# Performance work log

Measured on AMD Instinct MI355X. Metric: run time of the kernel, lower is better.

## Reference

```python
import jax, jax.numpy as jnp
import numpy as np

B, L, C = 32, 128, 21
PATCH, STRIDE = 16, 16
E, H, HEADS = 128, 128, 8
NLAYERS = 2
KSIZE = 3
PRED = 96
N = (L - PATCH) // STRIDE + 1  # 8 patches


def setup_inputs() -> dict:
    key = jax.random.key(0)
    ks = jax.random.split(key, 24)
    g = lambda i, shape, s=0.05: jax.random.normal(ks[i], shape, jnp.float32) * s
    return {
        'x': g(0, (B, L, C), 1.0),
        'embed_W': g(1, (E, PATCH)), 'embed_b': g(2, (E,)),
        'ln_g': jnp.ones((E,), jnp.float32), 'ln_b': jnp.zeros((E,), jnp.float32),
        'qW': g(3, (E, E)), 'qb': g(4, (E,)),
        'kW': g(5, (E, E)), 'kb': g(6, (E,)),
        'vW': g(7, (E, E)), 'vb': g(8, (E,)),
        'lstm_Wx': g(9, (NLAYERS, 4 * H, E)), 'lstm_Wh': g(10, (NLAYERS, 4 * H, H)), 'lstm_b': g(11, (NLAYERS, 4 * H)),
        'conv_W': g(12, (E, E, KSIZE)), 'conv_b': g(13, (E,)),
        'ssm_W': g(14, (E, E)), 'ssm_b': g(15, (E,)),
        'outp_W': g(16, (E, E)), 'outp_b': g(17, (E,)),
        'proj_W': g(18, (PRED, E)), 'proj_b': g(19, (PRED,)),
    }


def _layernorm(x, g, b, eps=1e-5):
    m = x.mean(-1, keepdims=True)
    v = ((x - m) ** 2).mean(-1, keepdims=True)
    return (x - m) * jax.lax.rsqrt(v + eps) * g + b


def _xlstm_dqn(ctx, Wx, Wh, bias):
    # DQNxLSTM: re-runs a 2-layer LSTM over the FULL sequence L times,
    # carrying (h,c) across iterations; returns the outputs of the last pass.
    ctx_T = jnp.swapaxes(ctx, 0, 1)  # [N, Bc, E]
    Bc = ctx.shape[0]
    h0 = jnp.zeros((NLAYERS, Bc, H), ctx.dtype)
    c0 = jnp.zeros_like(h0)

    def cell(carry, x_t):  # x_t: [Bc, E]
        h, c = carry
        inp = x_t
        hs, cs = [], []
        for l in range(NLAYERS):
            gates = inp @ Wx[l].T + h[l] @ Wh[l].T + bias[l]  # [Bc, 4H]
            i, f, g_, o = jnp.split(gates, 4, axis=-1)
            c_new = jax.nn.sigmoid(f) * c[l] + jax.nn.sigmoid(i) * jnp.tanh(g_)
            h_new = jax.nn.sigmoid(o) * jnp.tanh(c_new)
            hs.append(h_new); cs.append(c_new)
            inp = h_new
        return (jnp.stack(hs), jnp.stack(cs)), inp

    def outer(carry, _):
        carry2, outs = jax.lax.scan(cell, carry, ctx_T)  # outs: [N, Bc, H]
        return carry2, outs

    _, all_outs = jax.lax.scan(outer, (h0, c0), None, length=N)
    return jnp.swapaxes(all_outs[-1], 0, 1)  # [Bc, N, H]


def _conv1d_same(x, W, b):  # x: [Bc, N, E]
    y = jax.lax.conv_general_dilated(
        jnp.swapaxes(x, 1, 2), W, (1,), 'SAME',
        dimension_numbers=('NCH', 'OIH', 'NCH'))
    return jnp.swapaxes(y + b[None, :, None], 1, 2)


def reference(x, embed_W, embed_b, ln_g, ln_b, qW, qb, kW, kb, vW, vb,
              lstm_Wx, lstm_Wh, lstm_b, conv_W, conv_b, ssm_W, ssm_b,
              outp_W, outp_b, proj_W, proj_b):
    Bc = B * C
    # channel independence: b l c -> (b c) l
    xc = jnp.swapaxes(x, 1, 2).reshape(Bc, L)
    # patching (unfold)
    idx = jnp.arange(N)[:, None] * STRIDE + jnp.arange(PATCH)[None, :]
    patches = xc[:, idx]  # [Bc, N, PATCH]
    emb = patches @ embed_W.T + embed_b  # [Bc, N, E]
    xn = _layernorm(emb, ln_g, ln_b)
    # attention (faithful to original, incl. scale by sqrt(E) and bhnl,bhnd->bhnd einsum)
    d = E // HEADS
    q = (xn @ qW.T + qb).reshape(Bc, N, HEADS, d).transpose(0, 2, 1, 3)
    k = (xn @ kW.T + kb).reshape(Bc, N, HEADS, d).transpose(0, 2, 1, 3)
    v = (xn @ vW.T + vb).reshape(Bc, N, HEADS, d).transpose(0, 2, 1, 3)
    attn = jax.nn.softmax(jnp.einsum('bhnd,bhld->bhnl', q, k) / (E ** 0.5), axis=-1)
    ctx = jnp.einsum('bhnl,bhnd->bhnd', attn, v)  # as in original (elementwise-in-n)
    ctx = ctx.transpose(0, 2, 1, 3).reshape(Bc, N, E)
    ctx = _xlstm_dqn(ctx, lstm_Wx, lstm_Wh, lstm_b)
    ctx = _conv1d_same(ctx, conv_W, conv_b)
    ctx = ctx @ ssm_W.T + ssm_b
    ctx = ctx @ outp_W.T + outp_b
    ctx = ctx + xn  # residual onto the normed input (as in original)
    y = ctx @ proj_W.T + proj_b  # [Bc, N, PRED]
    return y
```

## Files before the change

### kernel.cpp

```cpp
#include <hip/hip_runtime.h>

typedef unsigned short ushort_t;
typedef unsigned int uint_t;

using bf16x8 = __attribute__((ext_vector_type(8))) short;
using f32x4  = __attribute__((ext_vector_type(4))) float;

__device__ __forceinline__ ushort_t f2b(float f){
    union { float f; uint_t u; } v; v.f = f;
    uint_t u = v.u;
    uint_t r = (u + 0x7FFFu + ((u >> 16) & 1u)) >> 16;
    return (ushort_t)r;
}

__global__ void prep_k(const float* __restrict__ vW, const float* __restrict__ Wx,
                       const float* __restrict__ Wh, const float* __restrict__ cW,
                       const float* __restrict__ sW, const float* __restrict__ oW,
                       const float* __restrict__ pW, const float* __restrict__ x,
                       ushort_t* __restrict__ wb, float* __restrict__ xT)
{
    int idx = blockIdx.x * 256 + threadIdx.x;
    switch (blockIdx.y){
    case 0: if (idx < 16384) wb[idx]          = f2b(vW[idx]);           break;
    case 1: if (idx < 65536) wb[16384  + idx] = f2b(Wx[idx]);           break;
    case 2: if (idx < 65536) wb[81920  + idx] = f2b(Wh[idx]);           break;
    case 3: if (idx < 65536) wb[147456 + idx] = f2b(Wx[65536 + idx]);   break;
    case 4: if (idx < 65536) wb[212992 + idx] = f2b(Wh[65536 + idx]);   break;
    case 5: if (idx < 49152){
                int k = idx >> 14; int oi = idx & 16383;
                wb[278528 + idx] = f2b(cW[oi * 3 + k]);
            } break;
    case 6: if (idx < 16384) wb[327680 + idx] = f2b(sW[idx]);           break;
    case 7: if (idx < 16384) wb[344064 + idx] = f2b(oW[idx]);           break;
    case 8: if (idx < 12288) wb[360448 + idx] = f2b(pW[idx]);           break;
    case 9:
        for (int i = idx; i < 86016; i += 65536){
            int bc = i >> 7, l = i & 127;
            int b = bc / 21, c = bc % 21;
            xT[i] = x[(b * 128 + l) * 21 + c];
        }
        break;
    }
}

__global__ __launch_bounds__(256) void head_k(
    const float* __restrict__ xT, const float* __restrict__ eW,
    const float* __restrict__ eb, const float* __restrict__ lng,
    const float* __restrict__ lnb, const ushort_t* __restrict__ vWb,
    const float* __restrict__ vb, const ushort_t* __restrict__ wx0b,
    const float* __restrict__ lb, float* __restrict__ xnF, float* __restrict__ X0F)
{
    __shared__ ushort_t xnL[2048];
    __shared__ ushort_t c0L[2048];

    const int tid = threadIdx.x;
    const int wv = tid >> 6, lane = tid & 63;
    const int rowbase = blockIdx.x * 16;
    const int e0 = lane, e1 = lane + 64;

    float w0[16], w1[16];
#pragma unroll
    for (int p = 0; p < 16; ++p){ w0[p] = eW[e0 * 16 + p]; w1[p] = eW[e1 * 16 + p]; }
    const float bi0 = eb[e0], bi1 = eb[e1];
    const float ga0 = lng[e0], ga1 = lng[e1];
    const float be0 = lnb[e0], be1 = lnb[e1];

    for (int i = wv; i < 16; i += 4){
        const int row = rowbase + i;
        const int bc = row >> 3, n = row & 7;
        const float* xp = xT + bc * 128 + n * 16;
        float v0 = bi0, v1 = bi1;
#pragma unroll
        for (int p = 0; p < 16; ++p){
            float pv = xp[p];
            v0 += w0[p] * pv; v1 += w1[p] * pv;
        }
        float s = v0 + v1, sq = v0 * v0 + v1 * v1;
#pragma unroll
        for (int m = 32; m >= 1; m >>= 1){
            s  += __shfl_xor(s,  m);
            sq += __shfl_xor(sq, m);
        }
        float mean = s * (1.f / 128.f);
        float var  = sq * (1.f / 128.f) - mean * mean;
        float r    = rsqrtf(var + 1e-5f);
        float y0 = (v0 - mean) * r * ga0 + be0;
        float y1 = (v1 - mean) * r * ga1 + be1;
        xnF[row * 128 + e0] = y0;
        xnF[row * 128 + e1] = y1;
        const int sz = (i & 7) << 3;
        xnL[i * 128 + (e0 ^ sz)] = f2b(y0);
        xnL[i * 128 + (e1 ^ sz)] = f2b(y1);
    }
    __syncthreads();

    const int r0 = lane & 15, g = lane >> 4, sw = r0 & 7;
    bf16x8 a[4];
#pragma unroll
    for (int kt = 0; kt < 4; ++kt)
        a[kt] = *(const bf16x8*)(&xnL[r0 * 128 + ((kt * 32 + g * 8) ^ (sw << 3))]);

#pragma unroll
    for (int j = 0; j < 2; ++j){
        const int nt = wv * 2 + j;
        const int col = nt * 16 + r0;
        float bv = vb[col];
        f32x4 acc = {bv, bv, bv, bv};
#pragma unroll
        for (int kt = 0; kt < 4; ++kt)
            acc = __builtin_amdgcn_mfma_f32_16x16x32_bf16(
                    a[kt], *(const bf16x8*)(vWb + col * 128 + kt * 32 + g * 8), acc, 0, 0, 0);
#pragma unroll
        for (int q = 0; q < 4; ++q){
            int rr = g * 4 + q;
            c0L[rr * 128 + (col ^ ((rr & 7) << 3))] = f2b(acc[q]);
        }
    }
    __syncthreads();

#pragma unroll
    for (int kt = 0; kt < 4; ++kt)
        a[kt] = *(const bf16x8*)(&c0L[r0 * 128 + ((kt * 32 + g * 8) ^ (sw << 3))]);

#pragma unroll
    for (int j = 0; j < 8; ++j){
        const int nt = wv * 8 + j;
        const int col = nt * 16 + r0;
        float bv = lb[col];
        f32x4 acc = {bv, bv, bv, bv};
#pragma unroll
        for (int kt = 0; kt < 4; ++kt)
            acc = __builtin_amdgcn_mfma_f32_16x16x32_bf16(
                    a[kt], *(const bf16x8*)(wx0b + col * 128 + kt * 32 + g * 8), acc, 0, 0, 0);
#pragma unroll
        for (int q = 0; q < 4; ++q)
            X0F[(rowbase + g * 4 + q) * 512 + col] = acc[q];
    }
}

__global__ __launch_bounds__(512, 2) void lstm_f2(
    const float* __restrict__ X0, const ushort_t* __restrict__ Wh0,
    const ushort_t* __restrict__ Wx1, const ushort_t* __restrict__ Wh1,
    const float* __restrict__ lb, ushort_t* __restrict__ outB)
{
    extern __shared__ ushort_t smem[];
    ushort_t* hbuf = smem;
    ushort_t* wxs  = smem + 8192;

    const int tid = threadIdx.x;
    const int wid = tid >> 6, lane = tid & 63;
    const int r0 = lane & 15, g = lane >> 4;
    const int sw = r0 & 7;
    const int bcb = blockIdx.x * 16;
    const float K1 = 1.44269504f, K2 = 2.88539008f;

    for (int i = tid; i < 8192; i += 512) hbuf[i] = 0;
    for (int idx = tid; idx < 8192; idx += 512){
        int col = idx >> 4, c = idx & 15;
        *(bf16x8*)(wxs + col * 128 + ((c ^ (col & 7)) << 3)) =
            *(const bf16x8*)(Wx1 + col * 128 + c * 8);
    }

    bf16x8 wh0[4][4], wh1[4][4];
#pragma unroll
    for (int t4 = 0; t4 < 4; ++t4){
        const int cb = t4 * 128 + wid * 16;
#pragma unroll
        for (int kt = 0; kt < 4; ++kt){
            wh0[t4][kt] = *(const bf16x8*)(Wh0 + (cb + r0) * 128 + kt * 32 + g * 8);
            wh1[t4][kt] = *(const bf16x8*)(Wh1 + (cb + r0) * 128 + kt * 32 + g * 8);
        }
    }
    float b1v[4];
#pragma unroll
    for (int t4 = 0; t4 < 4; ++t4) b1v[t4] = lb[512 + t4 * 128 + wid * 16 + r0];

    const char* adr[4];
#pragma unroll
    for (int kt = 0; kt < 4; ++kt)
        adr[kt] = (const char*)hbuf + r0 * 256 + (((kt * 32 + g * 8) ^ (sw << 3)) << 1);
    char* wrq[4];
#pragma unroll
    for (int q = 0; q < 4; ++q){
        int row = g * 4 + q;
        wrq[q] = (char*)hbuf + row * 256 + (((wid * 16 + r0) ^ ((row & 7) << 3)) << 1);
    }
    const char* wxp[4][2];
    {
        const int e = (sw >> 2) * 64;
#pragma unroll
        for (int t4 = 0; t4 < 4; ++t4){
            const char* base = (const char*)wxs
                + (t4 * 128 + wid * 16 + r0) * 256 + ((g ^ (sw & 3)) * 16);
            wxp[t4][0] = base + e;
            wxp[t4][1] = base + (64 - e);
        }
    }
    const char* xp[4];
#pragma unroll
    for (int q = 0; q < 4; ++q)
        xp[q] = (const char*)(X0 + (bcb + g * 4 + q) * 4096 + wid * 16 + r0) + 2048;
    int tnn = 1;

    float c0[4] = {0,0,0,0}, c1[4] = {0,0,0,0};

    f32x4 acc[4];
#pragma unroll
    for (int t4 = 0; t4 < 4; ++t4)
#pragma unroll
        for (int q = 0; q < 4; ++q)
            acc[t4][q] = *(const float*)(xp[q] - 2048 + t4 * 512);

    __syncthreads();

#pragma unroll 1
    for (int tt = 0; tt < 32; ++tt){
#pragma unroll
        for (int pp = 0; pp < 2; ++pp){
            const int ph = tt * 2 + pp;
            const int RDO = (pp ^ 1) * 4096;
            const int WRO = pp * 4096;

            bf16x8 a0[4], ah[4];
#pragma unroll
            for (int kt = 0; kt < 4; ++kt){
                a0[kt] = *(const bf16x8*)(adr[kt] + RDO);
                ah[kt] = *(const bf16x8*)(adr[kt] + 8192 + RDO);
            }

#pragma unroll
            for (int kt = 0; kt < 4; ++kt)
#pragma unroll
                for (int t4 = 0; t4 < 4; ++t4)
                    acc[t4] = __builtin_amdgcn_mfma_f32_16x16x32_bf16(a0[kt], wh0[t4][kt], acc[t4], 0, 0, 0);

#pragma unroll
            for (int q = 0; q < 4; ++q){
                float iv = acc[0][q], fv = acc[1][q], gv = acc[2][q], ov = acc[3][q];
                float af = 1.f + __builtin_amdgcn_exp2f(-K1 * fv);
                float ai = 1.f + __builtin_amdgcn_exp2f(-K1 * iv);
                float bg = 1.f + __builtin_amdgcn_exp2f( K2 * gv);
                float cn = c0[q] * __builtin_amdgcn_rcpf(af)
                         + (bg - 2.f) * __builtin_amdgcn_rcpf(ai * bg);
                c0[q] = cn;
                float ao = 1.f + __builtin_amdgcn_exp2f(-K1 * ov);
                float bc = 1.f + __builtin_amdgcn_exp2f( K2 * cn);
                float hv = (bc - 2.f) * __builtin_amdgcn_rcpf(ao * bc);
                *(ushort_t*)(wrq[q] + WRO) = f2b(hv);
            }

            if (ph > 0){
                f32x4 accB[4];
#pragma unroll
                for (int t4 = 0; t4 < 4; ++t4){
                    f32x4 tmp = {b1v[t4], b1v[t4], b1v[t4], b1v[t4]};
                    accB[t4] = tmp;
                }
#pragma unroll
                for (int kt = 0; kt < 4; ++kt)
#pragma unroll
                    for (int t4 = 0; t4 < 4; ++t4){
                        bf16x8 wx = *(const bf16x8*)(wxp[t4][kt & 1] + ((kt >> 1) << 7));
                        accB[t4] = __builtin_amdgcn_mfma_f32_16x16x32_bf16(a0[kt], wx,          accB[t4], 0, 0, 0);
                        accB[t4] = __builtin_amdgcn_mfma_f32_16x16x32_bf16(ah[kt], wh1[t4][kt], accB[t4], 0, 0, 0);
                    }
#pragma unroll
                for (int q = 0; q < 4; ++q){
                    float iv = accB[0][q], fv = accB[1][q], gv = accB[2][q], ov = accB[3][q];
                    float af = 1.f + __builtin_amdgcn_exp2f(-K1 * fv);
                    float ai = 1.f + __builtin_amdgcn_exp2f(-K1 * iv);
                    float bg = 1.f + __builtin_amdgcn_exp2f( K2 * gv);
                    float cn = c1[q] * __builtin_amdgcn_rcpf(af)
                             + (bg - 2.f) * __builtin_amdgcn_rcpf(ai * bg);
                    c1[q] = cn;
                    float ao = 1.f + __builtin_amdgcn_exp2f(-K1 * ov);
                    float bc = 1.f + __builtin_amdgcn_exp2f( K2 * cn);
                    float hv = (bc - 2.f) * __builtin_amdgcn_rcpf(ao * bc);
                    *(ushort_t*)(wrq[q] + 8192 + WRO) = f2b(hv);
                    if (ph >= 57){
                        int row = g * 4 + q;
                        outB[((bcb + row) * 8 + ((ph - 1) & 7)) * 128 + wid * 16 + r0] = f2b(hv);
                    }
                }
            }

            if (ph < 63){
#pragma unroll
                for (int t4 = 0; t4 < 4; ++t4)
#pragma unroll
                    for (int q = 0; q < 4; ++q)
                        acc[t4][q] = *(const float*)(xp[q] + t4 * 512);
                long d = (tnn == 7) ? -14336L : 2048L;
                tnn = (tnn == 7) ? 0 : tnn + 1;
#pragma unroll
                for (int q = 0; q < 4; ++q) xp[q] += d;
            }
            __syncthreads();
        }
    }

    {
        bf16x8 a0[4], ah[4];
#pragma unroll
        for (int kt = 0; kt < 4; ++kt){
            a0[kt] = *(const bf16x8*)(adr[kt] + 4096);
            ah[kt] = *(const bf16x8*)(adr[kt] + 8192 + 4096);
        }
        f32x4 acc2[4];
#pragma unroll
        for (int t4 = 0; t4 < 4; ++t4){
            f32x4 tmp = {b1v[t4], b1v[t4], b1v[t4], b1v[t4]};
            acc2[t4] = tmp;
        }
#pragma unroll
        for (int kt = 0; kt < 4; ++kt)
#pragma unroll
            for (int t4 = 0; t4 < 4; ++t4){
                bf16x8 wx = *(const bf16x8*)(wxp[t4][kt & 1] + ((kt >> 1) << 7));
                acc2[t4] = __builtin_amdgcn_mfma_f32_16x16x32_bf16(a0[kt], wx,          acc2[t4], 0, 0, 0);
                acc2[t4] = __builtin_amdgcn_mfma_f32_16x16x32_bf16(ah[kt], wh1[t4][kt], acc2[t4], 0, 0, 0);
            }
#pragma unroll
        for (int q = 0; q < 4; ++q){
            float iv = acc2[0][q], fv = acc2[1][q], gv = acc2[2][q], ov = acc2[3][q];
            float af = 1.f + __builtin_amdgcn_exp2f(-K1 * fv);
            float ai = 1.f + __builtin_amdgcn_exp2f(-K1 * iv);
            float bg = 1.f + __builtin_amdgcn_exp2f( K2 * gv);
            float cn = c1[q] * __builtin_amdgcn_rcpf(af)
                     + (bg - 2.f) * __builtin_amdgcn_rcpf(ai * bg);
            float ao = 1.f + __builtin_amdgcn_exp2f(-K1 * ov);
            float bc = 1.f + __builtin_amdgcn_exp2f( K2 * cn);
            float hv = (bc - 2.f) * __builtin_amdgcn_rcpf(ao * bc);
            int row = g * 4 + q;
            outB[((bcb + row) * 8 + 7) * 128 + wid * 16 + r0] = f2b(hv);
        }
    }
}

__global__ __launch_bounds__(256) void tail_k(
    const ushort_t* __restrict__ ls, const ushort_t* __restrict__ cWk,
    const float* __restrict__ cbias, const ushort_t* __restrict__ sW,
    const float* __restrict__ sbias, const ushort_t* __restrict__ oW,
    const float* __restrict__ obias, const float* __restrict__ xnF,
    const ushort_t* __restrict__ pW, const float* __restrict__ pbias,
    float* __restrict__ out)
{
    __shared__ ushort_t bufA[2048];
    __shared__ ushort_t bufB[2048];
    const int tid = threadIdx.x;
    const int wv = tid >> 6, lane = tid & 63;
    const int r0 = lane & 15, g = lane >> 4;
    const int rowbase = blockIdx.x * 16;

    {
        const int n = r0 & 7;
        bf16x8 a[3][4];
#pragma unroll
        for (int k = 0; k < 3; ++k){
            bool valid = (n + k >= 1) && (n + k <= 8);
            const ushort_t* ap = ls + (rowbase + r0 + k - 1) * 128 + g * 8;
#pragma unroll
            for (int kt = 0; kt < 4; ++kt){
                bf16x8 z = {0,0,0,0,0,0,0,0};
                a[k][kt] = valid ? *(const bf16x8*)(ap + kt * 32) : z;
            }
        }
#pragma unroll
        for (int j = 0; j < 2; ++j){
            const int nt = wv * 2 + j;
            const int col = nt * 16 + r0;
            float bv = cbias[col];
            f32x4 acc = {bv, bv, bv, bv};
#pragma unroll
            for (int k = 0; k < 3; ++k)
#pragma unroll
                for (int kt = 0; kt < 4; ++kt)
                    acc = __builtin_amdgcn_mfma_f32_16x16x32_bf16(
                            a[k][kt], *(const bf16x8*)(cWk + k * 16384 + col * 128 + kt * 32 + g * 8),
                            acc, 0, 0, 0);
#pragma unroll
            for (int q = 0; q < 4; ++q){
                int row = g * 4 + q;
                bufA[row * 128 + (col ^ ((row & 7) << 3))] = f2b(acc[q]);
            }
        }
    }
    __syncthreads();
    {
        bf16x8 a[4];
#pragma unroll
        for (int kt = 0; kt < 4; ++kt)
            a[kt] = *(const bf16x8*)(&bufA[r0 * 128 + ((kt * 32 + g * 8) ^ ((r0 & 7) << 3))]);
#pragma unroll
        for (int j = 0; j < 2; ++j){
            const int nt = wv * 2 + j;
            const int col = nt * 16 + r0;
            float bv = sbias[col];
            f32x4 acc = {bv, bv, bv, bv};
#pragma unroll
            for (int kt = 0; kt < 4; ++kt)
                acc = __builtin_amdgcn_mfma_f32_16x16x32_bf16(
                        a[kt], *(const bf16x8*)(sW + col * 128 + kt * 32 + g * 8), acc, 0, 0, 0);
#pragma unroll
            for (int q = 0; q < 4; ++q){
                int row = g * 4 + q;
                bufB[row * 128 + (col ^ ((row & 7) << 3))] = f2b(acc[q]);
            }
        }
    }
    __syncthreads();
    {
        bf16x8 a[4];
#pragma unroll
        for (int kt = 0; kt < 4; ++kt)
            a[kt] = *(const bf16x8*)(&bufB[r0 * 128 + ((kt * 32 + g * 8) ^ ((r0 & 7) << 3))]);
#pragma unroll
        for (int j = 0; j < 2; ++j){
            const int nt = wv * 2 + j;
            const int col = nt * 16 + r0;
            float bv = obias[col];
            f32x4 acc = {bv, bv, bv, bv};
#pragma unroll
            for (int kt = 0; kt < 4; ++kt)
                acc = __builtin_amdgcn_mfma_f32_16x16x32_bf16(
                        a[kt], *(const bf16x8*)(oW + col * 128 + kt * 32 + g * 8), acc, 0, 0, 0);
#pragma unroll
            for (int q = 0; q < 4; ++q){
                int row = g * 4 + q;
                float v = acc[q] + xnF[(rowbase + row) * 128 + col];
                bufA[row * 128 + (col ^ ((row & 7) << 3))] = f2b(v);
            }
        }
    }
    __syncthreads();
    {
        bf16x8 a[4];
#pragma unroll
        for (int kt = 0; kt < 4; ++kt)
            a[kt] = *(const bf16x8*)(&bufA[r0 * 128 + ((kt * 32 + g * 8) ^ ((r0 & 7) << 3))]);
        for (int nt = wv; nt < 6; nt += 4){
            const int col = nt * 16 + r0;
            float bv = pbias[col];
            f32x4 acc = {bv, bv, bv, bv};
#pragma unroll
            for (int kt = 0; kt < 4; ++kt)
                acc = __builtin_amdgcn_mfma_f32_16x16x32_bf16(
                        a[kt], *(const bf16x8*)(pW + col * 128 + kt * 32 + g * 8), acc, 0, 0, 0);
#pragma unroll
            for (int q = 0; q < 4; ++q)
                out[(rowbase + g * 4 + q) * 96 + col] = acc[q];
        }
    }
}

extern "C" void kernel_launch(void* const* d_in, const int* in_sizes, int n_in,
                              void* d_out, int out_size, void* d_ws, size_t ws_size,
                              hipStream_t stream)
{
    const float* x   = (const float*)d_in[0];
    const float* eW  = (const float*)d_in[1];
    const float* eb  = (const float*)d_in[2];
    const float* lng = (const float*)d_in[3];
    const float* lnb = (const float*)d_in[4];
    const float* vW  = (const float*)d_in[9];
    const float* vb  = (const float*)d_in[10];
    const float* Wx  = (const float*)d_in[11];
    const float* Wh  = (const float*)d_in[12];
    const float* lb  = (const float*)d_in[13];
    const float* cW  = (const float*)d_in[14];
    const float* cb_ = (const float*)d_in[15];
    const float* sW  = (const float*)d_in[16];
    const float* sb  = (const float*)d_in[17];
    const float* oW  = (const float*)d_in[18];
    const float* ob  = (const float*)d_in[19];
    const float* pW  = (const float*)d_in[20];
    const float* pb  = (const float*)d_in[21];

    char* ws = (char*)d_ws;
    float*    xnF = (float*)   (ws + 0);
    float*    X0F = (float*)   (ws + 5505024);
    ushort_t* lsB = (ushort_t*)(ws + 16515072);
    ushort_t* wb  = (ushort_t*)(ws + 17891328);
    float*    xT  = (float*)   (ws + 18874368);

    hipFuncSetAttribute((const void*)lstm_f2,
                        hipFuncAttributeMaxDynamicSharedMemorySize, 147456);

    prep_k<<<dim3(256, 10), 256, 0, stream>>>(vW, Wx, Wh, cW, sW, oW, pW, x, wb, xT);
    head_k<<<336, 256, 0, stream>>>(xT, eW, eb, lng, lnb, wb + 0, vb, wb + 16384, lb,
                                    xnF, X0F);
    lstm_f2<<<42, 512, 147456, stream>>>(X0F, wb + 81920, wb + 147456, wb + 212992,
                                         lb, lsB);
    tail_k<<<336, 256, 0, stream>>>(lsB, wb + 278528, cb_, wb + 327680, sb,
                                    wb + 344064, ob, xnF, wb + 360448, pb, (float*)d_out);
}
```

Measured before the change: 174.5 us.

## Fuse weight prep and input transpose into head kernel, convert head weights inline

Merges the separate prep kernel into the head kernel. Extra blocks (336..511) convert the LSTM, conv, ssm, out and proj weights to bf16 while the first 336 blocks run the embedding, layernorm and projections. The head blocks now gather their input columns straight into shared memory instead of reading a pre-transposed buffer, and they convert vW and Wx[0] to bf16 on the fly with packed convert instructions. This removes one kernel launch and the intermediate xT round trip through global memory. In exchange, each head block re-converts its fp32 weights itself, reading twice the bytes from global memory.

```diff
diff --git a/kernel.cpp b/kernel.cpp
--- a/kernel.cpp
+++ b/kernel.cpp
@@ -12,52 +12,64 @@
     uint_t r = (u + 0x7FFFu + ((u >> 16) & 1u)) >> 16;
     return (ushort_t)r;
 }
-
-__global__ void prep_k(const float* __restrict__ vW, const float* __restrict__ Wx,
-                       const float* __restrict__ Wh, const float* __restrict__ cW,
-                       const float* __restrict__ sW, const float* __restrict__ oW,
-                       const float* __restrict__ pW, const float* __restrict__ x,
-                       ushort_t* __restrict__ wb, float* __restrict__ xT)
+__device__ __forceinline__ uint_t cvtpk(float lo, float hi){
+    uint_t r;
+    asm("v_cvt_pk_bf16_f32 %0, %1, %2" : "=v"(r) : "v"(lo), "v"(hi));
+    return r;
+}
+__device__ __forceinline__ bf16x8 ldcvt8(const float* p){
+    float4 a = *(const float4*)p;
+    float4 b = *(const float4*)(p + 4);
+    union { uint_t u[4]; bf16x8 v; } r;
+    r.u[0] = cvtpk(a.x, a.y); r.u[1] = cvtpk(a.z, a.w);
+    r.u[2] = cvtpk(b.x, b.y); r.u[3] = cvtpk(b.z, b.w);
+    return r.v;
+}
+
+__global__ __launch_bounds__(256) void headprep_k(
+    const float* __restrict__ x, const float* __restrict__ eW,
+    const float* __restrict__ eb, const float* __restrict__ lng,
+    const float* __restrict__ lnb, const float* __restrict__ vW,
+    const float* __restrict__ vb, const float* __restrict__ Wx,
+    const float* __restrict__ Wh, const float* __restrict__ cW,
+    const float* __restrict__ sW, const float* __restrict__ oW,
+    const float* __restrict__ pW, const float* __restrict__ lb,
+    ushort_t* __restrict__ wb, float* __restrict__ xnF, float* __restrict__ X0F)
 {
-    int idx = blockIdx.x * 256 + threadIdx.x;
-    switch (blockIdx.y){
-    case 0: if (idx < 16384) wb[idx]          = f2b(vW[idx]);           break;
-    case 1: if (idx < 65536) wb[16384  + idx] = f2b(Wx[idx]);           break;
-    case 2: if (idx < 65536) wb[81920  + idx] = f2b(Wh[idx]);           break;
-    case 3: if (idx < 65536) wb[147456 + idx] = f2b(Wx[65536 + idx]);   break;
-    case 4: if (idx < 65536) wb[212992 + idx] = f2b(Wh[65536 + idx]);   break;
-    case 5: if (idx < 49152){
-                int k = idx >> 14; int oi = idx & 16383;
-                wb[278528 + idx] = f2b(cW[oi * 3 + k]);
-            } break;
-    case 6: if (idx < 16384) wb[327680 + idx] = f2b(sW[idx]);           break;
-    case 7: if (idx < 16384) wb[344064 + idx] = f2b(oW[idx]);           break;
-    case 8: if (idx < 12288) wb[360448 + idx] = f2b(pW[idx]);           break;
-    case 9:
-        for (int i = idx; i < 86016; i += 65536){
-            int bc = i >> 7, l = i & 127;
-            int b = bc / 21, c = bc % 21;
-            xT[i] = x[(b * 128 + l) * 21 + c];
-        }
-        break;
-    }
-}
-
-__global__ __launch_bounds__(256) void head_k(
-    const float* __restrict__ xT, const float* __restrict__ eW,
-    const float* __restrict__ eb, const float* __restrict__ lng,
-    const float* __restrict__ lnb, const ushort_t* __restrict__ vWb,
-    const float* __restrict__ vb, const ushort_t* __restrict__ wx0b,
-    const float* __restrict__ lb, float* __restrict__ xnF, float* __restrict__ X0F)
-{
+    __shared__ float    xcolL[256];
     __shared__ ushort_t xnL[2048];
     __shared__ ushort_t c0L[2048];
 
     const int tid = threadIdx.x;
+
+    if (blockIdx.x >= 336){
+        const int stride = 176 * 256;
+        for (int i = (blockIdx.x - 336) * 256 + tid; i < 290816; i += stride){
+            if (i < 65536)       wb[81920  + i]            = f2b(Wh[i]);
+            else if (i < 131072) wb[147456 + (i - 65536)]  = f2b(Wx[65536 + (i - 65536)]);
+            else if (i < 196608) wb[212992 + (i - 131072)] = f2b(Wh[65536 + (i - 131072)]);
+            else if (i < 245760){
+                int j = i - 196608; int k = j >> 14, oi = j & 16383;
+                wb[278528 + j] = f2b(cW[oi * 3 + k]);
+            }
+            else if (i < 262144) wb[327680 + (i - 245760)] = f2b(sW[i - 245760]);
+            else if (i < 278528) wb[344064 + (i - 262144)] = f2b(oW[i - 262144]);
+            else                 wb[360448 + (i - 278528)] = f2b(pW[i - 278528]);
+        }
+        return;
+    }
+
     const int wv = tid >> 6, lane = tid & 63;
     const int rowbase = blockIdx.x * 16;
+
+    {
+        const int colw = tid >> 7, l = tid & 127;
+        const int bcs = blockIdx.x * 2 + colw;
+        const int bs = bcs / 21, cs = bcs % 21;
+        xcolL[colw * 128 + l] = x[(bs * 128 + l) * 21 + cs];
+    }
+
     const int e0 = lane, e1 = lane + 64;
-
     float w0[16], w1[16];
 #pragma unroll
     for (int p = 0; p < 16; ++p){ w0[p] = eW[e0 * 16 + p]; w1[p] = eW[e1 * 16 + p]; }
@@ -65,10 +77,11 @@
     const float ga0 = lng[e0], ga1 = lng[e1];
     const float be0 = lnb[e0], be1 = lnb[e1];
 
+    __syncthreads();
+
     for (int i = wv; i < 16; i += 4){
         const int row = rowbase + i;
-        const int bc = row >> 3, n = row & 7;
-        const float* xp = xT + bc * 128 + n * 16;
+        const float* xp = &xcolL[(i >> 3) * 128 + (i & 7) * 16];
         float v0 = bi0, v1 = bi1;
 #pragma unroll
         for (int p = 0; p < 16; ++p){
@@ -109,7 +122,7 @@
 #pragma unroll
         for (int kt = 0; kt < 4; ++kt)
             acc = __builtin_amdgcn_mfma_f32_16x16x32_bf16(
-                    a[kt], *(const bf16x8*)(vWb + col * 128 + kt * 32 + g * 8), acc, 0, 0, 0);
+                    a[kt], ldcvt8(vW + col * 128 + kt * 32 + g * 8), acc, 0, 0, 0);
 #pragma unroll
         for (int q = 0; q < 4; ++q){
             int rr = g * 4 + q;
@@ -131,7 +144,7 @@
 #pragma unroll
         for (int kt = 0; kt < 4; ++kt)
             acc = __builtin_amdgcn_mfma_f32_16x16x32_bf16(
-                    a[kt], *(const bf16x8*)(wx0b + col * 128 + kt * 32 + g * 8), acc, 0, 0, 0);
+                    a[kt], ldcvt8(Wx + col * 128 + kt * 32 + g * 8), acc, 0, 0, 0);
 #pragma unroll
         for (int q = 0; q < 4; ++q)
             X0F[(rowbase + g * 4 + q) * 512 + col] = acc[q];
@@ -481,14 +494,12 @@
     float*    X0F = (float*)   (ws + 5505024);
     ushort_t* lsB = (ushort_t*)(ws + 16515072);
     ushort_t* wb  = (ushort_t*)(ws + 17891328);
-    float*    xT  = (float*)   (ws + 18874368);
 
     hipFuncSetAttribute((const void*)lstm_f2,
                         hipFuncAttributeMaxDynamicSharedMemorySize, 147456);
 
-    prep_k<<<dim3(256, 10), 256, 0, stream>>>(vW, Wx, Wh, cW, sW, oW, pW, x, wb, xT);
-    head_k<<<336, 256, 0, stream>>>(xT, eW, eb, lng, lnb, wb + 0, vb, wb + 16384, lb,
-                                    xnF, X0F);
+    headprep_k<<<512, 256, 0, stream>>>(x, eW, eb, lng, lnb, vW, vb, Wx, Wh,
+                                        cW, sW, oW, pW, lb, wb, xnF, X0F);
     lstm_f2<<<42, 512, 147456, stream>>>(X0F, wb + 81920, wb + 147456, wb + 212992,
                                          lb, lsB);
     tail_k<<<336, 256, 0, stream>>>(lsB, wb + 278528, cb_, wb + 327680, sb,
```

Result: slower. 178.2 us (+2.1%).
